# Kernel optimization log

Measured on AMD Instinct MI355X. Metric: run time of the kernel, lower is better.

Reference implementation:

```python
import jax, jax.numpy as jnp
import numpy as np

HIDDEN_DIM = 512  # H; hidden/encoder feature dim is 2H = 1024


def setup_inputs() -> dict:
    key = jax.random.key(0)
    k1, k2, k3, k4, k5 = jax.random.split(key, 5)
    B, S, D2, H = 16, 4096, 2 * HIDDEN_DIM, HIDDEN_DIM
    hidden = jax.random.normal(k1, (B, D2), dtype=jnp.float32)
    encoder_outputs = jax.random.normal(k2, (B, S, D2), dtype=jnp.float32)
    # nn.Linear(4H, H): weight [H, 4H] in torch; store transposed [4H, H] for x @ W
    W_attn = jax.random.normal(k3, (2 * D2, H), dtype=jnp.float32) * (1.0 / np.sqrt(2 * D2))
    b_attn = jax.random.normal(k4, (H,), dtype=jnp.float32) * 0.01
    # nn.Linear(H, 1, bias=False): weight [1, H] -> vector [H]
    w_v = jax.random.normal(k5, (H,), dtype=jnp.float32) * (1.0 / np.sqrt(H))
    return {"hidden": hidden, "encoder_outputs": encoder_outputs,
            "W_attn": W_attn, "b_attn": b_attn, "w_v": w_v}


def reference(hidden, encoder_outputs, W_attn, b_attn, w_v):
    B, S, D2 = encoder_outputs.shape
    # Broadcast decoder hidden over seq positions and concat with encoder outputs.
    hid = jnp.broadcast_to(hidden[:, None, :], (B, S, D2))
    cat = jnp.concatenate([hid, encoder_outputs], axis=2)        # [B, S, 4H]
    energy = jnp.tanh(cat @ W_attn + b_attn)                      # [B, S, H]
    scores = jnp.einsum('bsh,h->bs', energy, w_v)                 # [B, S]
    attention = jax.nn.softmax(scores, axis=1)                    # [B, S]
    context = jnp.einsum('bs,bsd->bd', attention, encoder_outputs)  # [B, 2H]
    return context
```

## Files before the change

### kernel.cpp

```cpp
#include <hip/hip_runtime.h>
#include <hip/hip_bf16.h>
#include <math.h>

#define HD   512
#define D2   1024
#define SEQ  4096
#define BAT  16
#define BM   128
#define BK   32
#define NKT  32

typedef _Float16 half8 __attribute__((ext_vector_type(8)));
typedef float    f32x4 __attribute__((ext_vector_type(4)));
typedef __attribute__((address_space(3))) void lds_void_t;
typedef __attribute__((address_space(1))) void glb_void_t;

__global__ void wconv_kernel(const float* __restrict__ W, _Float16* __restrict__ WtS) {
  __shared__ float tile[32][17];
  const int kt  = blockIdx.x;
  const int nbg = blockIdx.y;
  const int nh  = nbg >> 4, nbl = nbg & 15;
  const int t   = threadIdx.x;
  {
    const int n16 = t & 15, kk = t >> 4;
    #pragma unroll
    for (int i = 0; i < 2; ++i) {
      const int k = kk + i * 16;
      tile[k][n16] = W[(size_t)(D2 + kt * 32 + k) * HD + nh * 256 + nbl * 16 + n16];
    }
  }
  __syncthreads();
  if (t < 64) {
    const int kc = t >> 4, nlo = t & 15;
    half8 h;
    #pragma unroll
    for (int j = 0; j < 8; ++j) h[j] = (_Float16)tile[kc * 8 + j][nlo];
    *(half8*)(WtS + ((size_t)(kt * 2 + nh) * 1024 + nbl * 64 + kc * 16 + nlo) * 8) = h;
  }
}

__global__ void hproj_kernel(const float* __restrict__ hidden,
                             const float* __restrict__ W,
                             float* __restrict__ hproj) {
  const int b  = blockIdx.x >> 3;
  const int kc = blockIdx.x & 7;
  const int h  = threadIdx.x;
  float a0 = 0.f, a1 = 0.f;
  #pragma unroll 4
  for (int i = 0; i < 128; ++i) {
    const int d = kc * 128 + i;
    const float hd = hidden[b * D2 + d];
    a0 += hd * W[(size_t)d * HD + h];
    a1 += hd * W[(size_t)d * HD + h + 256];
  }
  atomicAdd(&hproj[b * HD + h], a0);
  atomicAdd(&hproj[b * HD + h + 256], a1);
}

__global__ __launch_bounds__(512, 2) void scores_kernel(
    const float* __restrict__ enc, const _Float16* __restrict__ WtS,
    const float* __restrict__ hproj, const float* __restrict__ b_attn,
    const float* __restrict__ w_v, float* __restrict__ scores)
{
  __shared__ __align__(16) float As[4][BM * BK];

  const int s0  = blockIdx.x * BM;
  const int b   = blockIdx.y;
  const int kt0 = (blockIdx.x + blockIdx.y) & 31;
  const int tid = threadIdx.x, lane = tid & 63, w = tid >> 6;
  const int col16 = lane & 15, q = lane >> 4;
  const int wm = w >> 2, wn = w & 3;

  const float* encB = enc + ((size_t)b * SEQ + s0) * D2;

  f32x4 acc[4][8];
  const f32x4 z = {0.f, 0.f, 0.f, 0.f};
  #pragma unroll
  for (int mi = 0; mi < 4; ++mi)
    #pragma unroll
    for (int ni = 0; ni < 8; ++ni) acc[mi][ni] = z;

  auto stageA = [&](int ktp, int buf) {
    const float* ek = encB + ktp * BK;
    #pragma unroll
    for (int i = 0; i < 2; ++i) {
      const int s = i * 512 + tid;
      const int row = s >> 3;
      const int g = (s & 7) ^ (row & 7);
      __builtin_amdgcn_global_load_lds((glb_void_t*)(ek + (size_t)row * D2 + g * 4),
          (lds_void_t*)((char*)&As[0][0] + (size_t)buf * 16384 + s * 16), 16, 0, 0);
    }
  };
  auto loadB = [&](int ktp, half8* bf) {
    const _Float16* wk = WtS + (size_t)ktp * 16384;
    #pragma unroll
    for (int ni = 0; ni < 8; ++ni)
      bf[ni] = *(const half8*)(wk + ((size_t)((wn * 8 + ni) * 64 + q * 16 + col16)) * 8);
  };
  auto compute = [&](int buf, const half8* bf) {
    const float* pA = &As[0][0] + (size_t)buf * 4096;
    half8 af[4];
    #pragma unroll
    for (int mi = 0; mi < 4; ++mi) {
      const int row = wm * 64 + mi * 16 + col16;
      const int rb = row * 8, rx = row & 7;
      const f32x4 lo = *(const f32x4*)&pA[(rb + ((2 * q)     ^ rx)) * 4];
      const f32x4 hi = *(const f32x4*)&pA[(rb + ((2 * q + 1) ^ rx)) * 4];
      half8 h;
      h[0] = (_Float16)lo[0]; h[1] = (_Float16)lo[1];
      h[2] = (_Float16)lo[2]; h[3] = (_Float16)lo[3];
      h[4] = (_Float16)hi[0]; h[5] = (_Float16)hi[1];
      h[6] = (_Float16)hi[2]; h[7] = (_Float16)hi[3];
      af[mi] = h;
    }
    __builtin_amdgcn_s_setprio(1);
    #pragma unroll
    for (int ni = 0; ni < 8; ++ni)
      #pragma unroll
      for (int mi = 0; mi < 4; ++mi)
        acc[mi][ni] = __builtin_amdgcn_mfma_f32_16x16x32_f16(af[mi], bf[ni], acc[mi][ni], 0, 0, 0);
    __builtin_amdgcn_s_setprio(0);
  };

  half8 BE[8], BO[8];

  stageA(kt0, 0);
  stageA((kt0 + 1) & 31, 1);
  stageA((kt0 + 2) & 31, 2);
  loadB(kt0, BE);

  for (int kt = 0; kt < 28; kt += 2) {
    loadB((kt + 1 + kt0) & 31, BO);
    __builtin_amdgcn_s_barrier();
    stageA((kt + 3 + kt0) & 31, (kt + 3) & 3);
    asm volatile("s_waitcnt vmcnt(12)" ::: "memory");
    compute(kt & 3, BE);

    loadB((kt + 2 + kt0) & 31, BE);
    __builtin_amdgcn_s_barrier();
    stageA((kt + 4 + kt0) & 31, (kt + 4) & 3);
    asm volatile("s_waitcnt vmcnt(12)" ::: "memory");
    compute((kt + 1) & 3, BO);
  }

  loadB((29 + kt0) & 31, BO);
  __builtin_amdgcn_s_barrier();
  stageA((31 + kt0) & 31, 3);
  asm volatile("s_waitcnt vmcnt(12)" ::: "memory");
  compute(0, BE);

  loadB((30 + kt0) & 31, BE);
  __builtin_amdgcn_s_barrier();
  asm volatile("s_waitcnt vmcnt(10)" ::: "memory");
  compute(1, BO);

  loadB((31 + kt0) & 31, BO);
  __builtin_amdgcn_s_barrier();
  asm volatile("s_waitcnt vmcnt(8)" ::: "memory");
  compute(2, BE);

  __builtin_amdgcn_s_barrier();
  asm volatile("s_waitcnt vmcnt(0)" ::: "memory");
  compute(3, BO);

  float p[4][4];
  #pragma unroll
  for (int mi = 0; mi < 4; ++mi)
    #pragma unroll
    for (int r = 0; r < 4; ++r) p[mi][r] = 0.f;

  #pragma unroll
  for (int ni = 0; ni < 8; ++ni) {
    const int n = wn * 128 + ni * 16 + col16;
    const float hb = hproj[b * HD + n] + b_attn[n];
    const float wv = w_v[n];
    #pragma unroll
    for (int mi = 0; mi < 4; ++mi) {
      #pragma unroll
      for (int r = 0; r < 4; ++r) {
        float x = fminf(fmaxf(acc[mi][ni][r] + hb, -15.f), 15.f);
        float ex = __expf(2.f * x);
        p[mi][r] += wv * __fdividef(ex - 1.f, ex + 1.f);
      }
    }
  }
  #pragma unroll
  for (int off = 8; off >= 1; off >>= 1) {
    #pragma unroll
    for (int mi = 0; mi < 4; ++mi)
      #pragma unroll
      for (int r = 0; r < 4; ++r)
        p[mi][r] += __shfl_xor(p[mi][r], off, 64);
  }

  float* red = (float*)&As[0][0];
  __syncthreads();
  if (col16 == 0) {
    #pragma unroll
    for (int mi = 0; mi < 4; ++mi)
      #pragma unroll
      for (int r = 0; r < 4; ++r)
        red[wn * 128 + wm * 64 + mi * 16 + q * 4 + r] = p[mi][r];
  }
  __syncthreads();
  if (tid < 128) {
    const float v = red[tid] + red[128 + tid] + red[256 + tid] + red[384 + tid];
    scores[b * SEQ + s0 + tid] = v;
  }
}

__global__ void softmax_kernel(float* __restrict__ scores) {
  const int b = blockIdx.x;
  float* sc = scores + b * SEQ;
  __shared__ float red[16];
  const int tid = threadIdx.x;
  float loc[16];
  float mx = -1e30f;
  #pragma unroll
  for (int i = 0; i < 16; ++i) { loc[i] = sc[i * 256 + tid]; mx = fmaxf(mx, loc[i]); }
  #pragma unroll
  for (int off = 32; off >= 1; off >>= 1) mx = fmaxf(mx, __shfl_xor(mx, off, 64));
  if ((tid & 63) == 0) red[tid >> 6] = mx;
  __syncthreads();
  mx = fmaxf(fmaxf(red[0], red[1]), fmaxf(red[2], red[3]));
  float sum = 0.f;
  #pragma unroll
  for (int i = 0; i < 16; ++i) { loc[i] = __expf(loc[i] - mx); sum += loc[i]; }
  #pragma unroll
  for (int off = 32; off >= 1; off >>= 1) sum += __shfl_xor(sum, off, 64);
  if ((tid & 63) == 0) red[8 + (tid >> 6)] = sum;
  __syncthreads();
  sum = red[8] + red[9] + red[10] + red[11];
  const float inv = 1.0f / sum;
  #pragma unroll
  for (int i = 0; i < 16; ++i) sc[i * 256 + tid] = loc[i] * inv;
}

__global__ __launch_bounds__(256) void context_kernel(const float* __restrict__ attn,
                                                      const float* __restrict__ enc,
                                                      float* __restrict__ out) {
  const int b  = blockIdx.y;
  const int s0 = blockIdx.x * 64;
  const int tid = threadIdx.x;
  const float* encB = enc + ((size_t)b * SEQ + s0) * D2 + tid * 4;
  const float* at   = attn + b * SEQ + s0;
  f32x4 acc0 = {0.f, 0.f, 0.f, 0.f}, acc1 = {0.f, 0.f, 0.f, 0.f};
  #pragma unroll 8
  for (int i = 0; i < 64; i += 2) {
    acc0 += at[i]     * *(const f32x4*)(encB + (size_t)i * D2);
    acc1 += at[i + 1] * *(const f32x4*)(encB + (size_t)(i + 1) * D2);
  }
  f32x4 acc = acc0 + acc1;
  float* o = out + b * D2 + tid * 4;
  atomicAdd(o + 0, acc[0]);
  atomicAdd(o + 1, acc[1]);
  atomicAdd(o + 2, acc[2]);
  atomicAdd(o + 3, acc[3]);
}

extern "C" void kernel_launch(void* const* d_in, const int* in_sizes, int n_in,
                              void* d_out, int out_size, void* d_ws, size_t ws_size,
                              hipStream_t stream) {
  (void)in_sizes; (void)n_in; (void)ws_size;
  const float* hidden = (const float*)d_in[0];
  const float* enc    = (const float*)d_in[1];
  const float* W      = (const float*)d_in[2];
  const float* b_attn = (const float*)d_in[3];
  const float* w_v    = (const float*)d_in[4];
  float* out = (float*)d_out;

  char* ws = (char*)d_ws;
  _Float16* WtS = (_Float16*)ws;
  float* hproj  = (float*)(ws + (1 << 20));
  float* scores = (float*)(ws + (1 << 20) + 32768);

  hipMemsetAsync(d_out, 0, (size_t)out_size * sizeof(float), stream);
  hipMemsetAsync(hproj, 0, BAT * HD * sizeof(float), stream);

  wconv_kernel  <<<dim3(32, 32),          256, 0, stream>>>(W, WtS);
  hproj_kernel  <<<dim3(128),             256, 0, stream>>>(hidden, W, hproj);
  scores_kernel <<<dim3(SEQ / BM, BAT),   512, 0, stream>>>(enc, WtS, hproj, b_attn, w_v, scores);
  softmax_kernel<<<dim3(BAT),             256, 0, stream>>>(scores);
  context_kernel<<<dim3(SEQ / 64, BAT),   256, 0, stream>>>(scores, enc, out);
}
```

Before: 470.0 us.

## Shrink scores tile to 32 rows and stage full encoder rows in LDS

The scores GEMM now uses 32-row tiles instead of 128. The full 32x1024 fp32 encoder slab is loaded into LDS once at kernel start, replacing the 4-stage rotating K pipeline. The eight waves now split only the N dimension, and the per-iteration barriers disappear because A is fully resident. In exchange, each block re-reads the whole fp16 weight matrix for 4x fewer rows, which raises weight traffic and cuts MFMA reuse. The 128KB LDS footprint also limits occupancy to one block per CU, and the initial encoder load no longer overlaps with compute.

```diff
diff --git a/kernel.cpp b/kernel.cpp
--- a/kernel.cpp
+++ b/kernel.cpp
@@ -6,8 +6,7 @@
 #define D2   1024
 #define SEQ  4096
 #define BAT  16
-#define BM   128
-#define BK   32
+#define BM   32
 #define NKT  32
 
 typedef _Float16 half8 __attribute__((ext_vector_type(8)));
@@ -62,50 +61,46 @@
     const float* __restrict__ hproj, const float* __restrict__ b_attn,
     const float* __restrict__ w_v, float* __restrict__ scores)
 {
-  __shared__ __align__(16) float As[4][BM * BK];
+  __shared__ __align__(16) float As[BM * 1024];
 
   const int s0  = blockIdx.x * BM;
   const int b   = blockIdx.y;
   const int kt0 = (blockIdx.x + blockIdx.y) & 31;
   const int tid = threadIdx.x, lane = tid & 63, w = tid >> 6;
   const int col16 = lane & 15, q = lane >> 4;
-  const int wm = w >> 2, wn = w & 3;
 
   const float* encB = enc + ((size_t)b * SEQ + s0) * D2;
 
-  f32x4 acc[4][8];
+  f32x4 acc[2][4];
   const f32x4 z = {0.f, 0.f, 0.f, 0.f};
   #pragma unroll
-  for (int mi = 0; mi < 4; ++mi)
-    #pragma unroll
-    for (int ni = 0; ni < 8; ++ni) acc[mi][ni] = z;
-
-  auto stageA = [&](int ktp, int buf) {
-    const float* ek = encB + ktp * BK;
-    #pragma unroll
-    for (int i = 0; i < 2; ++i) {
-      const int s = i * 512 + tid;
-      const int row = s >> 3;
-      const int g = (s & 7) ^ (row & 7);
-      __builtin_amdgcn_global_load_lds((glb_void_t*)(ek + (size_t)row * D2 + g * 4),
-          (lds_void_t*)((char*)&As[0][0] + (size_t)buf * 16384 + s * 16), 16, 0, 0);
-    }
-  };
+  for (int mi = 0; mi < 2; ++mi)
+    #pragma unroll
+    for (int ni = 0; ni < 4; ++ni) acc[mi][ni] = z;
+
+  #pragma unroll
+  for (int i = 0; i < 16; ++i) {
+    const int s = i * 512 + tid;
+    const int row = s >> 8, c = s & 255;
+    const int g = c ^ ((row & 7) << 1);
+    __builtin_amdgcn_global_load_lds((glb_void_t*)(encB + (size_t)row * D2 + g * 4),
+        (lds_void_t*)((char*)As + s * 16), 16, 0, 0);
+  }
+
   auto loadB = [&](int ktp, half8* bf) {
     const _Float16* wk = WtS + (size_t)ktp * 16384;
     #pragma unroll
-    for (int ni = 0; ni < 8; ++ni)
-      bf[ni] = *(const half8*)(wk + ((size_t)((wn * 8 + ni) * 64 + q * 16 + col16)) * 8);
+    for (int ni = 0; ni < 4; ++ni)
+      bf[ni] = *(const half8*)(wk + (size_t)((w * 4 + ni) * 64 + q * 16 + col16) * 8);
   };
-  auto compute = [&](int buf, const half8* bf) {
-    const float* pA = &As[0][0] + (size_t)buf * 4096;
-    half8 af[4];
-    #pragma unroll
-    for (int mi = 0; mi < 4; ++mi) {
-      const int row = wm * 64 + mi * 16 + col16;
-      const int rb = row * 8, rx = row & 7;
-      const f32x4 lo = *(const f32x4*)&pA[(rb + ((2 * q)     ^ rx)) * 4];
-      const f32x4 hi = *(const f32x4*)&pA[(rb + ((2 * q + 1) ^ rx)) * 4];
+  auto compute = [&](int ktp, const half8* bf) {
+    half8 af[2];
+    #pragma unroll
+    for (int mi = 0; mi < 2; ++mi) {
+      const int row = mi * 16 + col16;
+      const int ch = (ktp * 8 + q * 2) ^ ((row & 7) << 1);
+      const f32x4 lo = *(const f32x4*)&As[row * 1024 + ch * 4];
+      const f32x4 hi = *(const f32x4*)&As[row * 1024 + ch * 4 + 4];
       half8 h;
       h[0] = (_Float16)lo[0]; h[1] = (_Float16)lo[1];
       h[2] = (_Float16)lo[2]; h[3] = (_Float16)lo[3];
@@ -115,67 +110,45 @@
     }
     __builtin_amdgcn_s_setprio(1);
     #pragma unroll
-    for (int ni = 0; ni < 8; ++ni)
-      #pragma unroll
-      for (int mi = 0; mi < 4; ++mi)
+    for (int ni = 0; ni < 4; ++ni)
+      #pragma unroll
+      for (int mi = 0; mi < 2; ++mi)
         acc[mi][ni] = __builtin_amdgcn_mfma_f32_16x16x32_f16(af[mi], bf[ni], acc[mi][ni], 0, 0, 0);
     __builtin_amdgcn_s_setprio(0);
   };
 
-  half8 BE[8], BO[8];
-
-  stageA(kt0, 0);
-  stageA((kt0 + 1) & 31, 1);
-  stageA((kt0 + 2) & 31, 2);
+  half8 BE[4], BO[4];
+
   loadB(kt0, BE);
-
-  for (int kt = 0; kt < 28; kt += 2) {
+  __syncthreads();
+
+  for (int kt = 0; kt < 30; kt += 2) {
     loadB((kt + 1 + kt0) & 31, BO);
-    __builtin_amdgcn_s_barrier();
-    stageA((kt + 3 + kt0) & 31, (kt + 3) & 3);
-    asm volatile("s_waitcnt vmcnt(12)" ::: "memory");
-    compute(kt & 3, BE);
-
+    asm volatile("s_waitcnt vmcnt(4)" ::: "memory");
+    compute((kt + kt0) & 31, BE);
     loadB((kt + 2 + kt0) & 31, BE);
-    __builtin_amdgcn_s_barrier();
-    stageA((kt + 4 + kt0) & 31, (kt + 4) & 3);
-    asm volatile("s_waitcnt vmcnt(12)" ::: "memory");
-    compute((kt + 1) & 3, BO);
-  }
-
-  loadB((29 + kt0) & 31, BO);
-  __builtin_amdgcn_s_barrier();
-  stageA((31 + kt0) & 31, 3);
-  asm volatile("s_waitcnt vmcnt(12)" ::: "memory");
-  compute(0, BE);
-
-  loadB((30 + kt0) & 31, BE);
-  __builtin_amdgcn_s_barrier();
-  asm volatile("s_waitcnt vmcnt(10)" ::: "memory");
-  compute(1, BO);
-
+    asm volatile("s_waitcnt vmcnt(4)" ::: "memory");
+    compute((kt + 1 + kt0) & 31, BO);
+  }
   loadB((31 + kt0) & 31, BO);
-  __builtin_amdgcn_s_barrier();
-  asm volatile("s_waitcnt vmcnt(8)" ::: "memory");
-  compute(2, BE);
-
-  __builtin_amdgcn_s_barrier();
+  asm volatile("s_waitcnt vmcnt(4)" ::: "memory");
+  compute((30 + kt0) & 31, BE);
   asm volatile("s_waitcnt vmcnt(0)" ::: "memory");
-  compute(3, BO);
-
-  float p[4][4];
-  #pragma unroll
-  for (int mi = 0; mi < 4; ++mi)
+  compute((31 + kt0) & 31, BO);
+
+  float p[2][4];
+  #pragma unroll
+  for (int mi = 0; mi < 2; ++mi)
     #pragma unroll
     for (int r = 0; r < 4; ++r) p[mi][r] = 0.f;
 
   #pragma unroll
-  for (int ni = 0; ni < 8; ++ni) {
-    const int n = wn * 128 + ni * 16 + col16;
+  for (int ni = 0; ni < 4; ++ni) {
+    const int n = w * 64 + ni * 16 + col16;
     const float hb = hproj[b * HD + n] + b_attn[n];
     const float wv = w_v[n];
     #pragma unroll
-    for (int mi = 0; mi < 4; ++mi) {
+    for (int mi = 0; mi < 2; ++mi) {
       #pragma unroll
       for (int r = 0; r < 4; ++r) {
         float x = fminf(fmaxf(acc[mi][ni][r] + hb, -15.f), 15.f);
@@ -185,26 +158,27 @@
     }
   }
   #pragma unroll
-  for (int off = 8; off >= 1; off >>= 1) {
-    #pragma unroll
-    for (int mi = 0; mi < 4; ++mi)
+  for (int off = 1; off <= 8; off <<= 1) {
+    #pragma unroll
+    for (int mi = 0; mi < 2; ++mi)
       #pragma unroll
       for (int r = 0; r < 4; ++r)
         p[mi][r] += __shfl_xor(p[mi][r], off, 64);
   }
 
-  float* red = (float*)&As[0][0];
   __syncthreads();
   if (col16 == 0) {
     #pragma unroll
-    for (int mi = 0; mi < 4; ++mi)
+    for (int mi = 0; mi < 2; ++mi)
       #pragma unroll
       for (int r = 0; r < 4; ++r)
-        red[wn * 128 + wm * 64 + mi * 16 + q * 4 + r] = p[mi][r];
-  }
-  __syncthreads();
-  if (tid < 128) {
-    const float v = red[tid] + red[128 + tid] + red[256 + tid] + red[384 + tid];
+        As[w * 32 + mi * 16 + q * 4 + r] = p[mi][r];
+  }
+  __syncthreads();
+  if (tid < 32) {
+    float v = 0.f;
+    #pragma unroll
+    for (int j = 0; j < 8; ++j) v += As[j * 32 + tid];
     scores[b * SEQ + s0 + tid] = v;
   }
 }
```

New measurement: 527.3 us. 1.12x slower.
